# Kernel optimization log

Hardware: AMD Instinct MI355X
Metric: run time of the kernel (lower is better)

## Reference

```python
import jax, jax.numpy as jnp
import numpy as np

EPSILON = 0.001  # forward default in the torch module


def setup_inputs() -> dict:
    key = jax.random.key(0)
    z = jax.random.normal(key, (8192, 4096), dtype=jnp.float32)
    return {"z": z}


def reference(z):
    # Original: -mean(0.5 * logdet(lmbd * z_i z_i^T + I_D)) over batch.
    # Matrix determinant lemma: det(I + lmbd * v v^T) = 1 + lmbd * ||v||^2,
    # so logdet collapses to log1p(lmbd * sum(z_i^2)) — identical math.
    B, D = z.shape
    lmbd = jnp.asarray(D * (B * EPSILON), dtype=z.dtype)
    sq_norms = jnp.sum(z * z, axis=1)  # [B]
    return -0.5 * jnp.mean(jnp.log1p(lmbd * sq_norms))
```

## Files before the change

### kernel.cpp

```cpp
#include <hip/hip_runtime.h>

#define GTCR_EPS 0.001f
#define GTCR_D 4096

__global__ __launch_bounds__(256) void gtcr_row_kernel(
    const float* __restrict__ z, float* __restrict__ row_out, float lmbd) {
    const int row = blockIdx.x;
    const float4* zr = reinterpret_cast<const float4*>(z) + (size_t)row * (GTCR_D / 4);
    const int t = threadIdx.x;

    float4 v0 = zr[t];
    float4 v1 = zr[t + 256];
    float4 v2 = zr[t + 512];
    float4 v3 = zr[t + 768];

    float s0 = fmaf(v0.x, v0.x, fmaf(v0.y, v0.y, fmaf(v0.z, v0.z, v0.w * v0.w)));
    float s1 = fmaf(v1.x, v1.x, fmaf(v1.y, v1.y, fmaf(v1.z, v1.z, v1.w * v1.w)));
    float s2 = fmaf(v2.x, v2.x, fmaf(v2.y, v2.y, fmaf(v2.z, v2.z, v2.w * v2.w)));
    float s3 = fmaf(v3.x, v3.x, fmaf(v3.y, v3.y, fmaf(v3.z, v3.z, v3.w * v3.w)));
    float s = (s0 + s1) + (s2 + s3);

    #pragma unroll
    for (int off = 32; off > 0; off >>= 1)
        s += __shfl_down(s, off, 64);

    __shared__ float wsum[4];
    const int lane = threadIdx.x & 63;
    const int wid  = threadIdx.x >> 6;
    if (lane == 0) wsum[wid] = s;
    __syncthreads();
    if (threadIdx.x == 0) {
        float t4 = (wsum[0] + wsum[1]) + (wsum[2] + wsum[3]);
        row_out[row] = log1pf(lmbd * t4);
    }
}

__global__ __launch_bounds__(256) void gtcr_final_kernel(
    const float* __restrict__ row_vals, float* __restrict__ out, int B) {
    const float4* rv4 = reinterpret_cast<const float4*>(row_vals);
    const int n4 = B >> 2;
    float s = 0.0f;
    for (int i = threadIdx.x; i < n4; i += 256) {
        float4 v = rv4[i];
        s += (v.x + v.y) + (v.z + v.w);
    }

    #pragma unroll
    for (int off = 32; off > 0; off >>= 1)
        s += __shfl_down(s, off, 64);

    __shared__ float wsum[4];
    const int lane = threadIdx.x & 63;
    const int wid  = threadIdx.x >> 6;
    if (lane == 0) wsum[wid] = s;
    __syncthreads();
    if (threadIdx.x == 0) {
        float t = (wsum[0] + wsum[1]) + (wsum[2] + wsum[3]);
        out[0] = -0.5f * (t / (float)B);
    }
}

extern "C" void kernel_launch(void* const* d_in, const int* in_sizes, int n_in,
                              void* d_out, int out_size, void* d_ws, size_t ws_size,
                              hipStream_t stream) {
    const float* z = (const float*)d_in[0];
    float* out = (float*)d_out;
    float* row_vals = (float*)d_ws;

    const int B = in_sizes[0] / GTCR_D;
    const float lmbd = (float)GTCR_D * ((float)B * GTCR_EPS);

    gtcr_row_kernel<<<B, 256, 0, stream>>>(z, row_vals, lmbd);
    gtcr_final_kernel<<<1, 256, 0, stream>>>(row_vals, out, B);
}
```

Baseline: 29.00 us.

## Fuse row and final reductions via atomics with one wavefront per row

```diff
diff --git a/kernel.cpp b/kernel.cpp
--- a/kernel.cpp
+++ b/kernel.cpp
@@ -3,60 +3,48 @@
 #define GTCR_EPS 0.001f
 #define GTCR_D 4096
 
-__global__ __launch_bounds__(256) void gtcr_row_kernel(
-    const float* __restrict__ z, float* __restrict__ row_out, float lmbd) {
-    const int row = blockIdx.x;
+__global__ __launch_bounds__(256) void gtcr_fused_kernel(
+    const float* __restrict__ z, float* __restrict__ out,
+    float* __restrict__ acc, unsigned int* __restrict__ ctr,
+    float lmbd, int nblocks, float inv_B) {
+    const int wid  = threadIdx.x >> 6;
+    const int lane = threadIdx.x & 63;
+    const int row  = blockIdx.x * 4 + wid;
+
     const float4* zr = reinterpret_cast<const float4*>(z) + (size_t)row * (GTCR_D / 4);
-    const int t = threadIdx.x;
 
-    float4 v0 = zr[t];
-    float4 v1 = zr[t + 256];
-    float4 v2 = zr[t + 512];
-    float4 v3 = zr[t + 768];
-
-    float s0 = fmaf(v0.x, v0.x, fmaf(v0.y, v0.y, fmaf(v0.z, v0.z, v0.w * v0.w)));
-    float s1 = fmaf(v1.x, v1.x, fmaf(v1.y, v1.y, fmaf(v1.z, v1.z, v1.w * v1.w)));
-    float s2 = fmaf(v2.x, v2.x, fmaf(v2.y, v2.y, fmaf(v2.z, v2.z, v2.w * v2.w)));
-    float s3 = fmaf(v3.x, v3.x, fmaf(v3.y, v3.y, fmaf(v3.z, v3.z, v3.w * v3.w)));
+    float s0 = 0.0f, s1 = 0.0f, s2 = 0.0f, s3 = 0.0f;
+    #pragma unroll
+    for (int k = 0; k < 16; k += 4) {
+        float4 v0 = zr[lane + 64 * (k + 0)];
+        float4 v1 = zr[lane + 64 * (k + 1)];
+        float4 v2 = zr[lane + 64 * (k + 2)];
+        float4 v3 = zr[lane + 64 * (k + 3)];
+        s0 = fmaf(v0.x, v0.x, fmaf(v0.y, v0.y, fmaf(v0.z, v0.z, fmaf(v0.w, v0.w, s0))));
+        s1 = fmaf(v1.x, v1.x, fmaf(v1.y, v1.y, fmaf(v1.z, v1.z, fmaf(v1.w, v1.w, s1))));
+        s2 = fmaf(v2.x, v2.x, fmaf(v2.y, v2.y, fmaf(v2.z, v2.z, fmaf(v2.w, v2.w, s2))));
+        s3 = fmaf(v3.x, v3.x, fmaf(v3.y, v3.y, fmaf(v3.z, v3.z, fmaf(v3.w, v3.w, s3))));
+    }
     float s = (s0 + s1) + (s2 + s3);
 
     #pragma unroll
     for (int off = 32; off > 0; off >>= 1)
         s += __shfl_down(s, off, 64);
 
-    __shared__ float wsum[4];
-    const int lane = threadIdx.x & 63;
-    const int wid  = threadIdx.x >> 6;
-    if (lane == 0) wsum[wid] = s;
+    __shared__ float wres[4];
+    if (lane == 0) wres[wid] = log1pf(lmbd * s);
     __syncthreads();
+
     if (threadIdx.x == 0) {
-        float t4 = (wsum[0] + wsum[1]) + (wsum[2] + wsum[3]);
-        row_out[row] = log1pf(lmbd * t4);
-    }
-}
-
-__global__ __launch_bounds__(256) void gtcr_final_kernel(
-    const float* __restrict__ row_vals, float* __restrict__ out, int B) {
-    const float4* rv4 = reinterpret_cast<const float4*>(row_vals);
-    const int n4 = B >> 2;
-    float s = 0.0f;
-    for (int i = threadIdx.x; i < n4; i += 256) {
-        float4 v = rv4[i];
-        s += (v.x + v.y) + (v.z + v.w);
-    }
-
-    #pragma unroll
-    for (int off = 32; off > 0; off >>= 1)
-        s += __shfl_down(s, off, 64);
-
-    __shared__ float wsum[4];
-    const int lane = threadIdx.x & 63;
-    const int wid  = threadIdx.x >> 6;
-    if (lane == 0) wsum[wid] = s;
-    __syncthreads();
-    if (threadIdx.x == 0) {
-        float t = (wsum[0] + wsum[1]) + (wsum[2] + wsum[3]);
-        out[0] = -0.5f * (t / (float)B);
+        float bsum = (wres[0] + wres[1]) + (wres[2] + wres[3]);
+        atomicAdd(acc, bsum);
+        __threadfence();
+        unsigned int old = atomicAdd(ctr, 1u);
+        if (old == (unsigned int)(nblocks - 1)) {
+            __threadfence();
+            float total = atomicAdd(acc, 0.0f);
+            out[0] = -0.5f * total * inv_B;
+        }
     }
 }
 
@@ -65,11 +53,15 @@
                               hipStream_t stream) {
     const float* z = (const float*)d_in[0];
     float* out = (float*)d_out;
-    float* row_vals = (float*)d_ws;
 
     const int B = in_sizes[0] / GTCR_D;
+    const int nblocks = B / 4;
     const float lmbd = (float)GTCR_D * ((float)B * GTCR_EPS);
 
-    gtcr_row_kernel<<<B, 256, 0, stream>>>(z, row_vals, lmbd);
-    gtcr_final_kernel<<<1, 256, 0, stream>>>(row_vals, out, B);
+    float* acc = (float*)d_ws;
+    unsigned int* ctr = (unsigned int*)((char*)d_ws + 64);
+
+    hipMemsetAsync(d_ws, 0, 128, stream);
+    gtcr_fused_kernel<<<nblocks, 256, 0, stream>>>(
+        z, out, acc, ctr, lmbd, nblocks, 1.0f / (float)B);
 }
```

After: 92.66 us. 3.19x slower.
